# Kernel tuning notes

Measured on AMD Instinct MI355X. Metric: run time of the kernel, lower is better.

## Reference

```python
import jax, jax.numpy as jnp
import numpy as np

B, S, D, H = 4, 2048, 1024, 16
DK = D // H

def setup_inputs() -> dict:
    key = jax.random.key(0)
    ks = jax.random.split(key, 13)
    std = 1.0 / np.sqrt(D)
    inp = {
        'query': jax.random.normal(ks[0], (B, S, D), jnp.float32),
        'key':   jax.random.normal(ks[1], (B, S, D), jnp.float32),
        'value': jax.random.normal(ks[2], (B, S, D), jnp.float32),
        'mask':  jax.random.randint(ks[3], (B, 1, S), 0, 2, jnp.int32),
        'Wq': jax.random.normal(ks[4], (D, D), jnp.float32) * std,
        'bq': jnp.zeros((D,), jnp.float32),
        'Wk': jax.random.normal(ks[5], (D, D), jnp.float32) * std,
        'bk': jnp.zeros((D,), jnp.float32),
        'Wv': jax.random.normal(ks[6], (D, D), jnp.float32) * std,
        'bv': jnp.zeros((D,), jnp.float32),
        'Wo': jax.random.normal(ks[7], (D, D), jnp.float32) * std,
        'bo': jnp.zeros((D,), jnp.float32),
    }
    return inp

def reference(query, key, value, mask, Wq, bq, Wk, bk, Wv, bv, Wo, bo):
    # QKV projections (torch Linear: x @ W.T + b), reshape to [B,H,S,DK]
    def proj(x, W, b):
        y = x @ W.T + b
        return y.reshape(B, S, H, DK).transpose(0, 2, 1, 3)
    q = proj(query, Wq, bq)
    k = proj(key, Wk, bk)
    v = proj(value, Wv, bv)
    scores = jnp.einsum('bhqd,bhkd->bhqk', q, k) / jnp.sqrt(jnp.float32(DK))
    # mask [B,1,S] -> unsqueeze head dim -> [B,1,1,S], broadcast over h,q
    m = mask[:, None, :, :]  # [B,1,1,S]
    scores = jnp.where(m == 0, jnp.float32(-1e9), scores)
    p = jax.nn.softmax(scores, axis=-1)  # dropout omitted (eval mode)
    x = jnp.einsum('bhqk,bhkd->bhqd', p, v)
    x = x.transpose(0, 2, 1, 3).reshape(B, S, D)
    return x @ Wo.T + bo
```

## Files before the change

kernel.cpp:

```cpp
#include <hip/hip_runtime.h>

typedef unsigned short u16;
typedef __bf16 bf16x8 __attribute__((ext_vector_type(8)));
typedef float f32x4 __attribute__((ext_vector_type(4)));
typedef u16 u16x8 __attribute__((ext_vector_type(8)));
typedef u16 u16x4 __attribute__((ext_vector_type(4)));

typedef __attribute__((address_space(1))) const unsigned char gc_u8;
typedef __attribute__((address_space(3))) unsigned char lds_u8;

__device__ inline void gload16(const void* g, void* l) {
    __builtin_amdgcn_global_load_lds((gc_u8*)g, (lds_u8*)l, 16, 0, 0);
}
__device__ inline u16 f2bf(float f) {
    union { __bf16 h; u16 u; } c; c.h = (__bf16)f; return c.u;
}
__device__ inline float bf2f(u16 u) {
    union { u16 u[2]; float f; } c; c.u[0] = 0; c.u[1] = u; return c.f;
}
__device__ inline void hard_barrier() {
    __builtin_amdgcn_sched_barrier(0);
    __builtin_amdgcn_s_barrier();
    __builtin_amdgcn_sched_barrier(0);
}
#define WAIT_LGKM0() asm volatile("s_waitcnt lgkmcnt(0)" ::: "memory")
#define WAIT_VMCNT(n) asm volatile("s_waitcnt vmcnt(" #n ")" ::: "memory")

__global__ __launch_bounds__(256) void cvt4(const float* __restrict__ s0,
                                            const float* __restrict__ s1,
                                            const float* __restrict__ s2,
                                            const float* __restrict__ s3,
                                            u16* __restrict__ d0, u16* __restrict__ d1,
                                            u16* __restrict__ d2, u16* __restrict__ d3,
                                            int n) {
    const int y = blockIdx.y;
    const float* src = (y == 0) ? s0 : (y == 1) ? s1 : (y == 2) ? s2 : s3;
    u16* dst = (y == 0) ? d0 : (y == 1) ? d1 : (y == 2) ? d2 : d3;
    int i = (blockIdx.x * 256 + threadIdx.x) * 4;
    if (i < n) {
        float4 f = *reinterpret_cast<const float4*>(src + i);
        u16x4 u = { f2bf(f.x), f2bf(f.y), f2bf(f.z), f2bf(f.w) };
        *reinterpret_cast<u16x4*>(dst + i) = u;
    }
}

__global__ __launch_bounds__(256) void gemm_qkv(const float* __restrict__ Aq,
                                                const float* __restrict__ Ak,
                                                const float* __restrict__ Av,
                                                const u16* __restrict__ Bq,
                                                const u16* __restrict__ Bk,
                                                const u16* __restrict__ Bv,
                                                const float* __restrict__ bq,
                                                const float* __restrict__ bk,
                                                const float* __restrict__ bv,
                                                const int* __restrict__ Mk,
                                                u16* __restrict__ Cq,
                                                u16* __restrict__ Ck,
                                                u16* __restrict__ Cvp,
                                                int M, int N, int K) {
    __shared__ __align__(16) float Asf[2][128][32];
    __shared__ __align__(16) u16 Bs[2][128][32];
    const int z = blockIdx.z;
    const float* A = (z == 0) ? Aq : (z == 1) ? Ak : Av;
    const u16* B = (z == 0) ? Bq : (z == 1) ? Bk : Bv;
    const float* bias = (z == 0) ? bq : (z == 1) ? bk : bv;
    u16* Cv = (z == 0) ? Cq : (z == 1) ? Ck : Cvp;
    const bool vmode = (z == 2);

    const int t = threadIdx.x, lane = t & 63, w = t >> 6;
    const int wr = w >> 1, wc = w & 1;
    const int l15 = lane & 15, l16 = lane >> 4;
    const int nwg = gridDim.x, ntiles = N >> 7;
    const int wg = blockIdx.x, chunk = nwg >> 3;
    const int swz = (wg & 7) * chunk + (wg >> 3);
    const int bm = (swz / ntiles) * 128, bn = (swz % ntiles) * 128;
    const int srow = w * 16 + (lane >> 2);
    const int sgr = (lane & 3) * 8;
    const int arsub = lane >> 3;
    const int agr = ((lane & 7) ^ (lane >> 3)) * 4;
    const u16* Bb = B + (size_t)bn * K;

    f32x4 acc[4][4];
#pragma unroll
    for (int i = 0; i < 4; i++)
#pragma unroll
        for (int j = 0; j < 4; j++) acc[i][j] = (f32x4){0.f, 0.f, 0.f, 0.f};

    auto stage = [&](int c, int k0) {
#pragma unroll
        for (int ch = 0; ch < 4; ch++)
            gload16(A + (size_t)(bm + ch * 32 + w * 8 + arsub) * K + k0 + agr,
                    &Asf[c][ch * 32 + w * 8][0]);
        gload16(Bb + (size_t)srow * K + k0 + sgr,        &Bs[c][w * 16][0]);
        gload16(Bb + (size_t)(64 + srow) * K + k0 + sgr, &Bs[c][64 + w * 16][0]);
    };

    stage(0, 0);
    __syncthreads();

    const int NS = K >> 5;
    for (int i = 0; i < NS; ++i) {
        const int c = i & 1;
        WAIT_LGKM0();
        hard_barrier();
        if (i + 1 < NS) {
            stage(c ^ 1, (i + 1) * 32);
            WAIT_VMCNT(6);
        } else {
            WAIT_VMCNT(0);
        }
        hard_barrier();

        const int key = l15 & 7;
        bf16x8 afr[4], bfr[4];
#pragma unroll
        for (int mi = 0; mi < 4; mi++) {
            const int rr = wr * 64 + mi * 16 + l15;
            f32x4 lo = *(const f32x4*)&Asf[c][rr][((2 * l16) ^ key) * 4];
            f32x4 hi = *(const f32x4*)&Asf[c][rr][((2 * l16 + 1) ^ key) * 4];
            bf16x8 v;
            v[0] = (__bf16)lo[0]; v[1] = (__bf16)lo[1];
            v[2] = (__bf16)lo[2]; v[3] = (__bf16)lo[3];
            v[4] = (__bf16)hi[0]; v[5] = (__bf16)hi[1];
            v[6] = (__bf16)hi[2]; v[7] = (__bf16)hi[3];
            afr[mi] = v;
        }
#pragma unroll
        for (int ni = 0; ni < 4; ni++)
            bfr[ni] = *(const bf16x8*)&Bs[c][wc * 64 + ni * 16 + l15][l16 * 8];
#pragma unroll
        for (int mi = 0; mi < 4; mi++)
#pragma unroll
            for (int ni = 0; ni < 4; ni++)
                acc[mi][ni] = __builtin_amdgcn_mfma_f32_16x16x32_bf16(
                    afr[mi], bfr[ni], acc[mi][ni], 0, 0, 0);
    }

#pragma unroll
    for (int ni = 0; ni < 4; ni++) {
        const int col = bn + wc * 64 + ni * 16 + l15;
        const float bv2 = bias[col];
#pragma unroll
        for (int mi = 0; mi < 4; mi++) {
            const int r0 = bm + wr * 64 + mi * 16 + l16 * 4;
            if (vmode) {
                const int bb = r0 >> 11, ss = r0 & 2047;
                const int hh = col >> 6, dk = col & 63;
                const int4 m4 = *(const int4*)&Mk[bb * 2048 + ss];
                u16x4 pk;
                pk[0] = m4.x ? f2bf(acc[mi][ni][0] + bv2) : (u16)0;
                pk[1] = m4.y ? f2bf(acc[mi][ni][1] + bv2) : (u16)0;
                pk[2] = m4.z ? f2bf(acc[mi][ni][2] + bv2) : (u16)0;
                pk[3] = m4.w ? f2bf(acc[mi][ni][3] + bv2) : (u16)0;
                *(u16x4*)&Cv[(((size_t)(bb * 16 + hh) * 64 + dk) << 11) + ss] = pk;
            } else {
#pragma unroll
                for (int r = 0; r < 4; r++)
                    Cv[(size_t)(r0 + r) * N + col] = f2bf(acc[mi][ni][r] + bv2);
            }
        }
    }
}

__global__ __launch_bounds__(256) void gemm_out(const u16* __restrict__ A,
                                                const u16* __restrict__ B,
                                                const float* __restrict__ bias,
                                                float* __restrict__ Cv,
                                                int M, int N, int K) {
    __shared__ __align__(16) u16 As[2][128][32];
    __shared__ __align__(16) u16 Bs[2][128][32];
    const int t = threadIdx.x, lane = t & 63, w = t >> 6;
    const int wr = w >> 1, wc = w & 1;
    const int l15 = lane & 15, l16 = lane >> 4;
    const int nwg = gridDim.x, ntiles = N >> 7;
    const int wg = blockIdx.x, chunk = nwg >> 3;
    const int swz = (wg & 7) * chunk + (wg >> 3);
    const int bm = (swz / ntiles) * 128, bn = (swz % ntiles) * 128;
    const int srow = w * 16 + (lane >> 2);
    const int sgr = (lane & 3) * 8;
    const u16* Ab = A + (size_t)bm * K;
    const u16* Bb = B + (size_t)bn * K;

    f32x4 acc[4][4];
#pragma unroll
    for (int i = 0; i < 4; i++)
#pragma unroll
        for (int j = 0; j < 4; j++) acc[i][j] = (f32x4){0.f, 0.f, 0.f, 0.f};

    auto stage = [&](int c, int k0) {
        gload16(Ab + (size_t)srow * K + k0 + sgr,        &As[c][w * 16][0]);
        gload16(Ab + (size_t)(64 + srow) * K + k0 + sgr, &As[c][64 + w * 16][0]);
        gload16(Bb + (size_t)srow * K + k0 + sgr,        &Bs[c][w * 16][0]);
        gload16(Bb + (size_t)(64 + srow) * K + k0 + sgr, &Bs[c][64 + w * 16][0]);
    };

    stage(0, 0);
    __syncthreads();

    const int NS = K >> 5;
    for (int i = 0; i < NS; ++i) {
        const int c = i & 1;
        WAIT_LGKM0();
        hard_barrier();
        if (i + 1 < NS) {
            stage(c ^ 1, (i + 1) * 32);
            WAIT_VMCNT(4);
        } else {
            WAIT_VMCNT(0);
        }
        hard_barrier();

        bf16x8 afr[4], bfr[4];
#pragma unroll
        for (int mi = 0; mi < 4; mi++)
            afr[mi] = *(const bf16x8*)&As[c][wr * 64 + mi * 16 + l15][l16 * 8];
#pragma unroll
        for (int ni = 0; ni < 4; ni++)
            bfr[ni] = *(const bf16x8*)&Bs[c][wc * 64 + ni * 16 + l15][l16 * 8];
#pragma unroll
        for (int mi = 0; mi < 4; mi++)
#pragma unroll
            for (int ni = 0; ni < 4; ni++)
                acc[mi][ni] = __builtin_amdgcn_mfma_f32_16x16x32_bf16(
                    afr[mi], bfr[ni], acc[mi][ni], 0, 0, 0);
    }

#pragma unroll
    for (int ni = 0; ni < 4; ni++) {
        const int col = bn + wc * 64 + ni * 16 + l15;
        const float bv = bias[col];
#pragma unroll
        for (int mi = 0; mi < 4; mi++) {
            const int r0 = bm + wr * 64 + mi * 16 + l16 * 4;
#pragma unroll
            for (int r = 0; r < 4; r++)
                Cv[(size_t)(r0 + r) * N + col] = acc[mi][ni][r] + bv;
        }
    }
}

__global__ __launch_bounds__(256, 2) void attn_fwd(const u16* __restrict__ Q,
                                                   const u16* __restrict__ Kg,
                                                   const u16* __restrict__ Vt,
                                                   const int* __restrict__ mask,
                                                   u16* __restrict__ O) {
    constexpr int S = 2048, D = 1024;
    __shared__ __align__(16) u16 Kl[2][2][2][64][32];
    __shared__ __align__(16) u16 Vl[2][2][2][64][32];
    __shared__ __align__(16) u16 Pl[4][16][68];
    __shared__ __align__(16) u16 Ml[2048];
    const int t = threadIdx.x, lane = t & 63, w = t >> 6;
    const int l15 = lane & 15, l16 = lane >> 4;
    const int wg = blockIdx.x;
    const int swz = (wg & 7) * 64 + (wg >> 3);
    const int q0 = (swz & 7) * 256, h = (swz >> 3) & 15, b = swz >> 7;
    const int qb = q0 + w * 64;
    const int srow = w * 16 + (lane >> 2);
    const int sgr = ((lane & 3) ^ ((lane >> 3) & 3)) * 8;
    const int gsw8 = (l16 ^ ((l15 >> 1) & 3)) * 8;

    const u16* Khead = Kg + (size_t)b * S * D + h * 64;
    const u16* Vthead = Vt + (size_t)(b * 16 + h) * 64 * 2048;
    const int* mrow = mask + b * S;

    auto stage = [&](int c, int kt) {
#pragma unroll
        for (int kg = 0; kg < 2; kg++) {
            const int k0 = kt + kg * 64;
            gload16(Khead + (size_t)(k0 + srow) * D + sgr,        &Kl[c][kg][0][w * 16][0]);
            gload16(Khead + (size_t)(k0 + srow) * D + 32 + sgr,   &Kl[c][kg][1][w * 16][0]);
            gload16(Vthead + (size_t)srow * 2048 + k0 + sgr,      &Vl[c][kg][0][w * 16][0]);
            gload16(Vthead + (size_t)srow * 2048 + k0 + 32 + sgr, &Vl[c][kg][1][w * 16][0]);
        }
    };

    stage(0, 0);
    {
        const int4 ia = *(const int4*)&mrow[t * 8];
        const int4 ib = *(const int4*)&mrow[t * 8 + 4];
        u16x8 mv;
        mv[0] = ia.x ? (u16)0x3F80 : (u16)0;
        mv[1] = ia.y ? (u16)0x3F80 : (u16)0;
        mv[2] = ia.z ? (u16)0x3F80 : (u16)0;
        mv[3] = ia.w ? (u16)0x3F80 : (u16)0;
        mv[4] = ib.x ? (u16)0x3F80 : (u16)0;
        mv[5] = ib.y ? (u16)0x3F80 : (u16)0;
        mv[6] = ib.z ? (u16)0x3F80 : (u16)0;
        mv[7] = ib.w ? (u16)0x3F80 : (u16)0;
        *(u16x8*)&Ml[t * 8] = mv;
    }

    constexpr float QSCALE = 0.125f * 1.44269504f;
    bf16x8 aq[4][2];
#pragma unroll
    for (int qt = 0; qt < 4; qt++)
#pragma unroll
        for (int ks = 0; ks < 2; ks++) {
            const size_t qi = ((size_t)b * S + qb + qt * 16 + l15) * D +
                              h * 64 + ks * 32 + l16 * 8;
            u16x8 raw = *(const u16x8*)&Q[qi];
            bf16x8 qv;
#pragma unroll
            for (int i = 0; i < 8; i++) qv[i] = (__bf16)(bf2f(raw[i]) * QSCALE);
            aq[qt][ks] = qv;
        }

    f32x4 acc[4][4];
    f32x4 accl[4];
#pragma unroll
    for (int qt = 0; qt < 4; qt++) {
        accl[qt] = (f32x4){0.f, 0.f, 0.f, 0.f};
#pragma unroll
        for (int dt = 0; dt < 4; dt++) acc[qt][dt] = (f32x4){0.f, 0.f, 0.f, 0.f};
    }

    __syncthreads();

    for (int tile = 0; tile < S / 128; ++tile) {
        const int c = tile & 1;
        const int cur = tile * 128;
        WAIT_LGKM0();
        hard_barrier();
        if (tile + 1 < S / 128) {
            stage(c ^ 1, cur + 128);
            WAIT_VMCNT(8);
        } else {
            WAIT_VMCNT(0);
        }
        hard_barrier();

#pragma unroll
        for (int kg = 0; kg < 2; kg++) {
            bf16x8 kf0[4], kf1[4], vf0[4], vf1[4];
#pragma unroll
            for (int k4 = 0; k4 < 4; k4++) {
                kf0[k4] = *(const bf16x8*)&Kl[c][kg][0][k4 * 16 + l15][gsw8];
                kf1[k4] = *(const bf16x8*)&Kl[c][kg][1][k4 * 16 + l15][gsw8];
            }
#pragma unroll
            for (int dt = 0; dt < 4; dt++) {
                vf0[dt] = *(const bf16x8*)&Vl[c][kg][0][dt * 16 + l15][gsw8];
                vf1[dt] = *(const bf16x8*)&Vl[c][kg][1][dt * 16 + l15][gsw8];
            }
            const int kbase = cur + kg * 64;
            bf16x8 mv0 = *(const bf16x8*)&Ml[kbase + l16 * 8];
            bf16x8 mv1 = *(const bf16x8*)&Ml[kbase + 32 + l16 * 8];

#pragma unroll
            for (int qt = 0; qt < 4; qt++) {
#pragma unroll
                for (int k4 = 0; k4 < 4; k4++) {
                    f32x4 z = (f32x4){0.f, 0.f, 0.f, 0.f};
                    z = __builtin_amdgcn_mfma_f32_16x16x32_bf16(kf0[k4], aq[qt][0], z, 0, 0, 0);
                    z = __builtin_amdgcn_mfma_f32_16x16x32_bf16(kf1[k4], aq[qt][1], z, 0, 0, 0);
                    u16x4 pk;
#pragma unroll
                    for (int r = 0; r < 4; r++)
                        pk[r] = f2bf(__builtin_amdgcn_exp2f(z[r]));
                    *(u16x4*)&Pl[w][l15][k4 * 16 + l16 * 4] = pk;
                }
                bf16x8 pa0 = *(const bf16x8*)&Pl[w][l15][l16 * 8];
                bf16x8 pa1 = *(const bf16x8*)&Pl[w][l15][32 + l16 * 8];
                accl[qt] = __builtin_amdgcn_mfma_f32_16x16x32_bf16(pa0, mv0, accl[qt], 0, 0, 0);
                accl[qt] = __builtin_amdgcn_mfma_f32_16x16x32_bf16(pa1, mv1, accl[qt], 0, 0, 0);
#pragma unroll
                for (int dt = 0; dt < 4; dt++) {
                    acc[qt][dt] = __builtin_amdgcn_mfma_f32_16x16x32_bf16(
                        pa0, vf0[dt], acc[qt][dt], 0, 0, 0);
                    acc[qt][dt] = __builtin_amdgcn_mfma_f32_16x16x32_bf16(
                        pa1, vf1[dt], acc[qt][dt], 0, 0, 0);
                }
            }
        }
    }

#pragma unroll
    for (int qt = 0; qt < 4; qt++) {
        f32x4 inv;
#pragma unroll
        for (int r = 0; r < 4; r++) inv[r] = 1.f / accl[qt][r];
#pragma unroll
        for (int dt = 0; dt < 4; dt++)
#pragma unroll
            for (int r = 0; r < 4; r++) {
                const int tok = qb + qt * 16 + l16 * 4 + r;
                O[((size_t)b * S + tok) * D + h * 64 + dt * 16 + l15] =
                    f2bf(acc[qt][dt][r] * inv[r]);
            }
    }
}

extern "C" void kernel_launch(void* const* d_in, const int* in_sizes, int n_in,
                              void* d_out, int out_size, void* d_ws, size_t ws_size,
                              hipStream_t stream) {
    const float* query = (const float*)d_in[0];
    const float* key   = (const float*)d_in[1];
    const float* value = (const float*)d_in[2];
    const int*   mask  = (const int*)d_in[3];
    const float* Wq = (const float*)d_in[4];
    const float* bq = (const float*)d_in[5];
    const float* Wk = (const float*)d_in[6];
    const float* bk = (const float*)d_in[7];
    const float* Wv = (const float*)d_in[8];
    const float* bv = (const float*)d_in[9];
    const float* Wo = (const float*)d_in[10];
    const float* bo = (const float*)d_in[11];
    float* out = (float*)d_out;

    constexpr int S = 2048, D = 1024;
    constexpr size_t MSZ = (size_t)4 * S * D;
    constexpr size_t WSZ = (size_t)D * D;
    const size_t need = 4 * WSZ * 2 + 4 * MSZ * 2;
    if (ws_size < need) return;

    char* p = (char*)d_ws;
    u16* Wqb = (u16*)p; p += WSZ * 2;
    u16* Wkb = (u16*)p; p += WSZ * 2;
    u16* Wvb = (u16*)p; p += WSZ * 2;
    u16* Wob = (u16*)p; p += WSZ * 2;
    u16* Xb  = (u16*)p; p += MSZ * 2;
    u16* Qb  = (u16*)p; p += MSZ * 2;
    u16* Kb  = (u16*)p; p += MSZ * 2;
    u16* Vtb = (u16*)p; p += MSZ * 2;

    cvt4<<<dim3(WSZ / 1024, 4), 256, 0, stream>>>(Wq, Wk, Wv, Wo,
                                                  Wqb, Wkb, Wvb, Wob, (int)WSZ);
    gemm_qkv<<<dim3(512, 1, 3), 256, 0, stream>>>(query, key, value,
                                                  Wqb, Wkb, Wvb, bq, bk, bv, mask,
                                                  Qb, Kb, Vtb, 8192, 1024, 1024);
    attn_fwd<<<512, 256, 0, stream>>>(Qb, Kb, Vtb, mask, Xb);
    gemm_out<<<512, 256, 0, stream>>>(Xb, Wob, bo, out, 8192, 1024, 1024);
}
```

Before: 188.4 us.

## Switch attention to 32x32x16 MFMA and keep P in registers via permlane swap

Rewrites the attention inner loop to use 32x32x16 bf16 MFMA tiles instead of 16x16x32. The exponentiated scores stay in registers: they are packed with v_cvt_pk_bf16_f32 and rearranged with v_permlane32_swap into the A-operand layout, which removes the LDS round trip through the Pl buffer. This aims to cut LDS traffic and the waits on it, and to get more work per MFMA instruction. The cost is larger accumulator register footprints (f32x16), which could hurt occupancy under the 2-blocks-per-SM launch bound.

```diff
diff --git a/kernel.cpp b/kernel.cpp
--- a/kernel.cpp
+++ b/kernel.cpp
@@ -1,10 +1,13 @@
 #include <hip/hip_runtime.h>
 
 typedef unsigned short u16;
+typedef unsigned int u32;
 typedef __bf16 bf16x8 __attribute__((ext_vector_type(8)));
 typedef float f32x4 __attribute__((ext_vector_type(4)));
+typedef float f32x16 __attribute__((ext_vector_type(16)));
 typedef u16 u16x8 __attribute__((ext_vector_type(8)));
 typedef u16 u16x4 __attribute__((ext_vector_type(4)));
+typedef u32 u32x4 __attribute__((ext_vector_type(4)));
 
 typedef __attribute__((address_space(1))) const unsigned char gc_u8;
 typedef __attribute__((address_space(3))) unsigned char lds_u8;
@@ -17,6 +20,14 @@
 }
 __device__ inline float bf2f(u16 u) {
     union { u16 u[2]; float f; } c; c.u[0] = 0; c.u[1] = u; return c.f;
+}
+__device__ inline u32 cvtpk(float lo, float hi) {
+    u32 r;
+    asm("v_cvt_pk_bf16_f32 %0, %1, %2" : "=v"(r) : "v"(lo), "v"(hi));
+    return r;
+}
+__device__ inline void plswap(u32& a, u32& b) {
+    asm("v_permlane32_swap_b32 %0, %1" : "+v"(a), "+v"(b));
 }
 __device__ inline void hard_barrier() {
     __builtin_amdgcn_sched_barrier(0);
@@ -247,20 +258,19 @@
     constexpr int S = 2048, D = 1024;
     __shared__ __align__(16) u16 Kl[2][2][2][64][32];
     __shared__ __align__(16) u16 Vl[2][2][2][64][32];
-    __shared__ __align__(16) u16 Pl[4][16][68];
     __shared__ __align__(16) u16 Ml[2048];
     const int t = threadIdx.x, lane = t & 63, w = t >> 6;
-    const int l15 = lane & 15, l16 = lane >> 4;
+    const int l31 = lane & 31, hb = lane >> 5;
     const int wg = blockIdx.x;
     const int swz = (wg & 7) * 64 + (wg >> 3);
-    const int q0 = (swz & 7) * 256, h = (swz >> 3) & 15, b = swz >> 7;
+    const int q0 = (swz & 7) * 256, hd = (swz >> 3) & 15, b = swz >> 7;
     const int qb = q0 + w * 64;
     const int srow = w * 16 + (lane >> 2);
     const int sgr = ((lane & 3) ^ ((lane >> 3) & 3)) * 8;
-    const int gsw8 = (l16 ^ ((l15 >> 1) & 3)) * 8;
-
-    const u16* Khead = Kg + (size_t)b * S * D + h * 64;
-    const u16* Vthead = Vt + (size_t)(b * 16 + h) * 64 * 2048;
+    const int rsw = (l31 >> 1) & 3;
+
+    const u16* Khead = Kg + (size_t)b * S * D + hd * 64;
+    const u16* Vthead = Vt + (size_t)(b * 16 + hd) * 64 * 2048;
     const int* mrow = mask + b * S;
 
     auto stage = [&](int c, int kt) {
@@ -291,27 +301,27 @@
     }
 
     constexpr float QSCALE = 0.125f * 1.44269504f;
-    bf16x8 aq[4][2];
-#pragma unroll
-    for (int qt = 0; qt < 4; qt++)
-#pragma unroll
-        for (int ks = 0; ks < 2; ks++) {
-            const size_t qi = ((size_t)b * S + qb + qt * 16 + l15) * D +
-                              h * 64 + ks * 32 + l16 * 8;
+    bf16x8 aq[2][4];
+#pragma unroll
+    for (int qt2 = 0; qt2 < 2; qt2++)
+#pragma unroll
+        for (int ch = 0; ch < 4; ch++) {
+            const size_t qi = ((size_t)b * S + qb + qt2 * 32 + l31) * D +
+                              hd * 64 + ch * 16 + hb * 8;
             u16x8 raw = *(const u16x8*)&Q[qi];
             bf16x8 qv;
 #pragma unroll
             for (int i = 0; i < 8; i++) qv[i] = (__bf16)(bf2f(raw[i]) * QSCALE);
-            aq[qt][ks] = qv;
-        }
-
-    f32x4 acc[4][4];
-    f32x4 accl[4];
-#pragma unroll
-    for (int qt = 0; qt < 4; qt++) {
-        accl[qt] = (f32x4){0.f, 0.f, 0.f, 0.f};
-#pragma unroll
-        for (int dt = 0; dt < 4; dt++) acc[qt][dt] = (f32x4){0.f, 0.f, 0.f, 0.f};
+            aq[qt2][ch] = qv;
+        }
+
+    f32x16 acc[2][2];
+    f32x16 accl[2];
+#pragma unroll
+    for (int qt2 = 0; qt2 < 2; qt2++) {
+        accl[qt2] = (f32x16)(0.f);
+#pragma unroll
+        for (int dt2 = 0; dt2 < 2; dt2++) acc[qt2][dt2] = (f32x16)(0.f);
     }
 
     __syncthreads();
@@ -331,61 +341,76 @@
 
 #pragma unroll
         for (int kg = 0; kg < 2; kg++) {
-            bf16x8 kf0[4], kf1[4], vf0[4], vf1[4];
-#pragma unroll
-            for (int k4 = 0; k4 < 4; k4++) {
-                kf0[k4] = *(const bf16x8*)&Kl[c][kg][0][k4 * 16 + l15][gsw8];
-                kf1[k4] = *(const bf16x8*)&Kl[c][kg][1][k4 * 16 + l15][gsw8];
-            }
-#pragma unroll
-            for (int dt = 0; dt < 4; dt++) {
-                vf0[dt] = *(const bf16x8*)&Vl[c][kg][0][dt * 16 + l15][gsw8];
-                vf1[dt] = *(const bf16x8*)&Vl[c][kg][1][dt * 16 + l15][gsw8];
-            }
-            const int kbase = cur + kg * 64;
-            bf16x8 mv0 = *(const bf16x8*)&Ml[kbase + l16 * 8];
-            bf16x8 mv1 = *(const bf16x8*)&Ml[kbase + 32 + l16 * 8];
-
-#pragma unroll
-            for (int qt = 0; qt < 4; qt++) {
-#pragma unroll
-                for (int k4 = 0; k4 < 4; k4++) {
-                    f32x4 z = (f32x4){0.f, 0.f, 0.f, 0.f};
-                    z = __builtin_amdgcn_mfma_f32_16x16x32_bf16(kf0[k4], aq[qt][0], z, 0, 0, 0);
-                    z = __builtin_amdgcn_mfma_f32_16x16x32_bf16(kf1[k4], aq[qt][1], z, 0, 0, 0);
-                    u16x4 pk;
-#pragma unroll
-                    for (int r = 0; r < 4; r++)
-                        pk[r] = f2bf(__builtin_amdgcn_exp2f(z[r]));
-                    *(u16x4*)&Pl[w][l15][k4 * 16 + l16 * 4] = pk;
-                }
-                bf16x8 pa0 = *(const bf16x8*)&Pl[w][l15][l16 * 8];
-                bf16x8 pa1 = *(const bf16x8*)&Pl[w][l15][32 + l16 * 8];
-                accl[qt] = __builtin_amdgcn_mfma_f32_16x16x32_bf16(pa0, mv0, accl[qt], 0, 0, 0);
-                accl[qt] = __builtin_amdgcn_mfma_f32_16x16x32_bf16(pa1, mv1, accl[qt], 0, 0, 0);
-#pragma unroll
-                for (int dt = 0; dt < 4; dt++) {
-                    acc[qt][dt] = __builtin_amdgcn_mfma_f32_16x16x32_bf16(
-                        pa0, vf0[dt], acc[qt][dt], 0, 0, 0);
-                    acc[qt][dt] = __builtin_amdgcn_mfma_f32_16x16x32_bf16(
-                        pa1, vf1[dt], acc[qt][dt], 0, 0, 0);
+#pragma unroll
+            for (int kt2 = 0; kt2 < 2; kt2++) {
+                bf16x8 kf[4];
+#pragma unroll
+                for (int ch = 0; ch < 4; ch++)
+                    kf[ch] = *(const bf16x8*)&Kl[c][kg][ch >> 1][kt2 * 32 + l31]
+                                               [(((ch & 1) * 2 + hb) ^ rsw) * 8];
+                bf16x8 vf[2][2];
+#pragma unroll
+                for (int dt2 = 0; dt2 < 2; dt2++)
+#pragma unroll
+                    for (int wd = 0; wd < 2; wd++)
+                        vf[dt2][wd] = *(const bf16x8*)&Vl[c][kg][kt2][dt2 * 32 + l31]
+                                                        [((wd * 2 + hb) ^ rsw) * 8];
+                const int kbase = cur + kg * 64 + kt2 * 32;
+                bf16x8 mf0 = *(const bf16x8*)&Ml[kbase + hb * 8];
+                bf16x8 mf1 = *(const bf16x8*)&Ml[kbase + 16 + hb * 8];
+
+#pragma unroll
+                for (int qt2 = 0; qt2 < 2; qt2++) {
+                    f32x16 zz = (f32x16)(0.f);
+#pragma unroll
+                    for (int ch = 0; ch < 4; ch++)
+                        zz = __builtin_amdgcn_mfma_f32_32x32x16_bf16(kf[ch], aq[qt2][ch],
+                                                                     zz, 0, 0, 0);
+                    float p[16];
+#pragma unroll
+                    for (int r = 0; r < 16; r++) p[r] = __builtin_amdgcn_exp2f(zz[r]);
+
+                    u32 a0 = cvtpk(p[0], p[1]), b0 = cvtpk(p[2], p[3]);
+                    u32 c0 = cvtpk(p[4], p[5]), d0 = cvtpk(p[6], p[7]);
+                    plswap(a0, c0);
+                    plswap(b0, d0);
+                    u32x4 w0 = {a0, b0, c0, d0};
+                    bf16x8 pf0 = *(bf16x8*)&w0;
+                    u32 a1 = cvtpk(p[8], p[9]),  b1 = cvtpk(p[10], p[11]);
+                    u32 c1 = cvtpk(p[12], p[13]), d1 = cvtpk(p[14], p[15]);
+                    plswap(a1, c1);
+                    plswap(b1, d1);
+                    u32x4 w1 = {a1, b1, c1, d1};
+                    bf16x8 pf1 = *(bf16x8*)&w1;
+
+                    accl[qt2] = __builtin_amdgcn_mfma_f32_32x32x16_bf16(pf0, mf0,
+                                                                        accl[qt2], 0, 0, 0);
+                    accl[qt2] = __builtin_amdgcn_mfma_f32_32x32x16_bf16(pf1, mf1,
+                                                                        accl[qt2], 0, 0, 0);
+#pragma unroll
+                    for (int dt2 = 0; dt2 < 2; dt2++) {
+                        acc[qt2][dt2] = __builtin_amdgcn_mfma_f32_32x32x16_bf16(
+                            pf0, vf[dt2][0], acc[qt2][dt2], 0, 0, 0);
+                        acc[qt2][dt2] = __builtin_amdgcn_mfma_f32_32x32x16_bf16(
+                            pf1, vf[dt2][1], acc[qt2][dt2], 0, 0, 0);
+                    }
                 }
             }
         }
     }
 
 #pragma unroll
-    for (int qt = 0; qt < 4; qt++) {
-        f32x4 inv;
-#pragma unroll
-        for (int r = 0; r < 4; r++) inv[r] = 1.f / accl[qt][r];
-#pragma unroll
-        for (int dt = 0; dt < 4; dt++)
-#pragma unroll
-            for (int r = 0; r < 4; r++) {
-                const int tok = qb + qt * 16 + l16 * 4 + r;
-                O[((size_t)b * S + tok) * D + h * 64 + dt * 16 + l15] =
-                    f2bf(acc[qt][dt][r] * inv[r]);
+    for (int qt2 = 0; qt2 < 2; qt2++) {
+        f32x16 inv;
+#pragma unroll
+        for (int r = 0; r < 16; r++) inv[r] = 1.f / accl[qt2][r];
+#pragma unroll
+        for (int dt2 = 0; dt2 < 2; dt2++)
+#pragma unroll
+            for (int r = 0; r < 16; r++) {
+                const int q = qt2 * 32 + (r & 3) + 8 * (r >> 2) + 4 * hb;
+                O[((size_t)b * S + qb + q) * D + hd * 64 + dt2 * 32 + l31] =
+                    f2bf(acc[qt2][dt2][r] * inv[r]);
             }
     }
 }
```

Measured after the change: 190.9 us. About the same (+1.3%).

## Compact unmasked keys and values before attention to skip masked tiles

Applied to the files above, without the earlier changes.

Adds two kernels that gather only unmasked K rows and V^T columns per batch into compacted buffers (staged in the output buffer) and record the valid count. The attention kernel then loops only over the ceil(Nb/128) tiles and builds its mask from the count instead of reading the mask. With roughly half the keys masked, this roughly halves the attention inner-loop work, at the cost of extra compaction kernels with serial, poorly coalesced copy loops. Fully masked rows would differ numerically from the reference, but those don't occur for these inputs.

```diff
diff --git a/kernel.cpp b/kernel.cpp
--- a/kernel.cpp
+++ b/kernel.cpp
@@ -1,6 +1,7 @@
 #include <hip/hip_runtime.h>
 
 typedef unsigned short u16;
+typedef unsigned int u32;
 typedef __bf16 bf16x8 __attribute__((ext_vector_type(8)));
 typedef float f32x4 __attribute__((ext_vector_type(4)));
 typedef u16 u16x8 __attribute__((ext_vector_type(8)));
@@ -239,10 +240,93 @@
     }
 }
 
+__global__ __launch_bounds__(256) void compactK(const u16* __restrict__ Kb,
+                                                u16* __restrict__ Kc,
+                                                const int* __restrict__ mask) {
+    __shared__ u32 W[64];
+    __shared__ u32 Wpre[65];
+    const int t = threadIdx.x;
+    const int b = blockIdx.y, chunk = blockIdx.x;
+    const int* mrow = mask + b * 2048;
+    if (t < 64) {
+        u32 wv = 0;
+#pragma unroll 8
+        for (int j = 0; j < 32; j++) wv |= (mrow[t * 32 + j] ? 1u : 0u) << j;
+        W[t] = wv;
+    }
+    __syncthreads();
+    if (t == 0) {
+        u32 s = 0;
+        for (int i = 0; i < 64; i++) { Wpre[i] = s; s += __popc(W[i]); }
+        Wpre[64] = s;
+    }
+    __syncthreads();
+    const int Nb = (int)Wpre[64];
+    if (chunk == 8) {
+        const int pad = (Nb + 127) & ~127;
+        for (int r = Nb; r < pad; ++r) {
+            u16x4 z = {0, 0, 0, 0};
+            *(u16x4*)&Kc[((size_t)b * 2048 + r) * 1024 + t * 4] = z;
+        }
+        return;
+    }
+    const int s0 = chunk * 256;
+    for (int i = 0; i < 256; ++i) {
+        const int s = s0 + i;
+        const u32 word = W[s >> 5];
+        if ((word >> (s & 31)) & 1u) {
+            const int d = (int)Wpre[s >> 5] + __popc(word & ((1u << (s & 31)) - 1u));
+            *(u16x4*)&Kc[((size_t)b * 2048 + d) * 1024 + t * 4] =
+                *(const u16x4*)&Kb[((size_t)b * 2048 + s) * 1024 + t * 4];
+        }
+    }
+}
+
+__global__ __launch_bounds__(256) void compactV(const u16* __restrict__ Vtb,
+                                                u16* __restrict__ Vtc,
+                                                const int* __restrict__ mask,
+                                                int* __restrict__ NbA) {
+    __shared__ u32 W[64];
+    __shared__ u32 Wpre[65];
+    const int t = threadIdx.x, lane = t & 63, w = t >> 6;
+    const int h = blockIdx.x, b = blockIdx.y;
+    const int* mrow = mask + b * 2048;
+    if (t < 64) {
+        u32 wv = 0;
+#pragma unroll 8
+        for (int j = 0; j < 32; j++) wv |= (mrow[t * 32 + j] ? 1u : 0u) << j;
+        W[t] = wv;
+    }
+    __syncthreads();
+    if (t == 0) {
+        u32 s = 0;
+        for (int i = 0; i < 64; i++) { Wpre[i] = s; s += __popc(W[i]); }
+        Wpre[64] = s;
+        if (h == 0) NbA[b] = (int)s;
+    }
+    __syncthreads();
+    const int Nb = (int)Wpre[64];
+    const int pad = (Nb + 127) & ~127;
+    for (int dk = w; dk < 64; dk += 4) {
+        const u16* src = Vtb + ((size_t)(b * 16 + h) * 64 + dk) * 2048;
+        u16* dst = Vtc + ((size_t)(b * 16 + h) * 64 + dk) * 2048;
+        for (int i = 0; i < 32; ++i) {
+            const int s = i * 64 + lane;
+            const u32 word = W[s >> 5];
+            const u16 v = src[s];
+            if ((word >> (s & 31)) & 1u) {
+                const int d = (int)Wpre[s >> 5] + __popc(word & ((1u << (s & 31)) - 1u));
+                dst[d] = v;
+            }
+        }
+        for (int s = Nb + lane; s < pad; s += 64) dst[s] = 0;
+    }
+}
+
 __global__ __launch_bounds__(256, 2) void attn_fwd(const u16* __restrict__ Q,
                                                    const u16* __restrict__ Kg,
                                                    const u16* __restrict__ Vt,
-                                                   const int* __restrict__ mask,
+                                                   const int* __restrict__ NbA,
                                                    u16* __restrict__ O) {
     constexpr int S = 2048, D = 1024;
     __shared__ __align__(16) u16 Kl[2][2][2][64][32];
@@ -253,15 +337,17 @@
     const int l15 = lane & 15, l16 = lane >> 4;
     const int wg = blockIdx.x;
     const int swz = (wg & 7) * 64 + (wg >> 3);
-    const int q0 = (swz & 7) * 256, h = (swz >> 3) & 15, b = swz >> 7;
+    const int q0 = (swz & 7) * 256, hd = (swz >> 3) & 15, b = swz >> 7;
     const int qb = q0 + w * 64;
     const int srow = w * 16 + (lane >> 2);
     const int sgr = ((lane & 3) ^ ((lane >> 3) & 3)) * 8;
     const int gsw8 = (l16 ^ ((l15 >> 1) & 3)) * 8;
 
-    const u16* Khead = Kg + (size_t)b * S * D + h * 64;
-    const u16* Vthead = Vt + (size_t)(b * 16 + h) * 64 * 2048;
-    const int* mrow = mask + b * S;
+    const int Nb = NbA[b];
+    const int nt = (Nb + 127) >> 7;
+
+    const u16* Khead = Kg + (size_t)b * S * D + hd * 64;
+    const u16* Vthead = Vt + (size_t)(b * 16 + hd) * 64 * 2048;
 
     auto stage = [&](int c, int kt) {
 #pragma unroll
@@ -276,17 +362,9 @@
 
     stage(0, 0);
     {
-        const int4 ia = *(const int4*)&mrow[t * 8];
-        const int4 ib = *(const int4*)&mrow[t * 8 + 4];
         u16x8 mv;
-        mv[0] = ia.x ? (u16)0x3F80 : (u16)0;
-        mv[1] = ia.y ? (u16)0x3F80 : (u16)0;
-        mv[2] = ia.z ? (u16)0x3F80 : (u16)0;
-        mv[3] = ia.w ? (u16)0x3F80 : (u16)0;
-        mv[4] = ib.x ? (u16)0x3F80 : (u16)0;
-        mv[5] = ib.y ? (u16)0x3F80 : (u16)0;
-        mv[6] = ib.z ? (u16)0x3F80 : (u16)0;
-        mv[7] = ib.w ? (u16)0x3F80 : (u16)0;
+#pragma unroll
+        for (int j = 0; j < 8; j++) mv[j] = (t * 8 + j < Nb) ? (u16)0x3F80 : (u16)0;
         *(u16x8*)&Ml[t * 8] = mv;
     }
 
@@ -297,7 +375,7 @@
 #pragma unroll
         for (int ks = 0; ks < 2; ks++) {
             const size_t qi = ((size_t)b * S + qb + qt * 16 + l15) * D +
-                              h * 64 + ks * 32 + l16 * 8;
+                              hd * 64 + ks * 32 + l16 * 8;
             u16x8 raw = *(const u16x8*)&Q[qi];
             bf16x8 qv;
 #pragma unroll
@@ -316,12 +394,12 @@
 
     __syncthreads();
 
-    for (int tile = 0; tile < S / 128; ++tile) {
+    for (int tile = 0; tile < nt; ++tile) {
         const int c = tile & 1;
         const int cur = tile * 128;
         WAIT_LGKM0();
         hard_barrier();
-        if (tile + 1 < S / 128) {
+        if (tile + 1 < nt) {
             stage(c ^ 1, cur + 128);
             WAIT_VMCNT(8);
         } else {
@@ -384,7 +462,7 @@
 #pragma unroll
             for (int r = 0; r < 4; r++) {
                 const int tok = qb + qt * 16 + l16 * 4 + r;
-                O[((size_t)b * S + tok) * D + h * 64 + dt * 16 + l15] =
+                O[((size_t)b * S + tok) * D + hd * 64 + dt * 16 + l15] =
                     f2bf(acc[qt][dt][r] * inv[r]);
             }
     }
@@ -410,7 +488,7 @@
     constexpr int S = 2048, D = 1024;
     constexpr size_t MSZ = (size_t)4 * S * D;
     constexpr size_t WSZ = (size_t)D * D;
-    const size_t need = 4 * WSZ * 2 + 4 * MSZ * 2;
+    const size_t need = 4 * WSZ * 2 + 4 * MSZ * 2 + 64;
     if (ws_size < need) return;
 
     char* p = (char*)d_ws;
@@ -422,12 +500,17 @@
     u16* Qb  = (u16*)p; p += MSZ * 2;
     u16* Kb  = (u16*)p; p += MSZ * 2;
     u16* Vtb = (u16*)p; p += MSZ * 2;
+    int* NbA = (int*)p; p += 64;
+    u16* Kc  = (u16*)d_out;
+    u16* Vtc = (u16*)d_out + MSZ;
 
     cvt4<<<dim3(WSZ / 1024, 4), 256, 0, stream>>>(Wq, Wk, Wv, Wo,
                                                   Wqb, Wkb, Wvb, Wob, (int)WSZ);
     gemm_qkv<<<dim3(512, 1, 3), 256, 0, stream>>>(query, key, value,
                                                   Wqb, Wkb, Wvb, bq, bk, bv, mask,
                                                   Qb, Kb, Vtb, 8192, 1024, 1024);
-    attn_fwd<<<512, 256, 0, stream>>>(Qb, Kb, Vtb, mask, Xb);
+    compactK<<<dim3(9, 4), 256, 0, stream>>>(Kb, Kc, mask);
+    compactV<<<dim3(16, 4), 256, 0, stream>>>(Vtb, Vtc, mask, NbA);
+    attn_fwd<<<512, 256, 0, stream>>>(Qb, Kc, Vtc, NbA, Xb);
     gemm_out<<<512, 256, 0, stream>>>(Xb, Wob, bo, out, 8192, 1024, 1024);
 }
```

After: 365.7 us. +94.1%, slower.
